# Performance work log

Hardware: AMD Instinct MI355X
Metric: run time of the kernel (lower is better)

The kernel has to match this reference:

```python
import jax, jax.numpy as jnp
from jax import lax
import numpy as np

B = 512      # instances
C = 64       # cases (segments)
HID = 1024
ATT = 128


def _conv(x, w, b):
    # torch Conv2d(kernel=5, padding=2), NCHW / OIHW layout
    y = lax.conv_general_dilated(x, w, (1, 1), [(2, 2), (2, 2)],
                                 dimension_numbers=('NCHW', 'OIHW', 'NCHW'))
    return y + b[None, :, None, None]


def _pool(x):
    # MaxPool2d(2)
    return lax.reduce_window(x, -jnp.inf, lax.max, (1, 1, 2, 2), (1, 1, 2, 2), 'VALID')


def setup_inputs() -> dict:
    key = jax.random.key(0)
    ks = jax.random.split(key, 20)

    def rn(k, shape, scale=0.05):
        return jax.random.normal(k, shape, dtype=jnp.float32) * scale

    inp = {
        'data': jax.random.normal(ks[0], (B, 3, 128, 128), dtype=jnp.float32),
        'case_ids': jnp.sort(jax.random.randint(ks[1], (B,), 0, C, dtype=jnp.int32)),
    }
    chans = [(3, 8), (8, 16), (16, 32), (32, 64), (64, 128)]
    for i, (ci, co) in enumerate(chans):
        inp[f'conv_w{i + 1}'] = rn(ks[2 + 2 * i], (co, ci, 5, 5))
        inp[f'conv_b{i + 1}'] = jnp.zeros((co,), jnp.float32)
    inp['fc_w'] = rn(ks[12], (HID, 128 * 4 * 4), 0.02)
    inp['fc_b'] = jnp.zeros((HID,), jnp.float32)
    inp['att_w1'] = rn(ks[13], (ATT, HID), 0.02)
    inp['att_b1'] = jnp.zeros((ATT,), jnp.float32)
    inp['att_w2'] = rn(ks[14], (1, ATT), 0.02)
    inp['att_b2'] = jnp.zeros((1,), jnp.float32)
    inp['clf_w'] = rn(ks[15], (1, HID), 0.02)
    inp['clf_b'] = jnp.zeros((1,), jnp.float32)
    return inp


def reference(data, case_ids, conv_w1, conv_b1, conv_w2, conv_b2, conv_w3, conv_b3,
              conv_w4, conv_b4, conv_w5, conv_b5, fc_w, fc_b,
              att_w1, att_b1, att_w2, att_b2, clf_w, clf_b):
    x = data
    for w, b in ((conv_w1, conv_b1), (conv_w2, conv_b2), (conv_w3, conv_b3),
                 (conv_w4, conv_b4), (conv_w5, conv_b5)):
        x = jax.nn.relu(_pool(_conv(x, w, b)))
    emb = x.reshape(x.shape[0], -1) @ fc_w.T + fc_b          # (B, HID)

    # --- segment (per-case) attention pooling, vectorized over all cases ---
    logits = (jnp.tanh(emb @ att_w1.T + att_b1) @ att_w2.T + att_b2)[:, 0]  # (B,)
    seg_max = jax.ops.segment_max(logits, case_ids, num_segments=C)
    seg_max = jnp.where(jnp.isfinite(seg_max), seg_max, 0.0)  # guard empty segments
    e = jnp.exp(logits - lax.stop_gradient(seg_max)[case_ids])
    denom = jax.ops.segment_sum(e, case_ids, num_segments=C)
    wgt = e / denom[case_ids]                                  # segment softmax
    aggr = jax.ops.segment_sum(wgt[:, None] * emb, case_ids, num_segments=C)  # (C, HID)

    # --- classifier ---
    return jax.nn.sigmoid(aggr @ clf_w.T + clf_b)              # (C, 1)
```

## Files before the change

### kernel.cpp

```cpp
#include <hip/hip_runtime.h>
#include <hip/hip_bf16.h>
#include <math.h>

#define BATCH 512
#define NSEG  64
#define HID   1024
#define ATT   128

typedef __attribute__((ext_vector_type(8))) __bf16 bf16x8;
typedef __attribute__((ext_vector_type(4))) __bf16 bf16x4;
typedef __attribute__((ext_vector_type(4))) float  f32x4;

__global__ void wconv1_k(const float* __restrict__ w, __bf16* __restrict__ wt) {
    int t = blockIdx.x * 256 + threadIdx.x;
    if (t >= 2048) return;
    int j = t & 7, m = (t >> 3) & 15, k8 = t >> 7;
    int k = k8 * 8 + j, tap = k >> 2, ci = k & 3;
    float v = 0.f;
    if (m < 8 && ci < 3 && tap < 25) v = w[(m * 3 + ci) * 25 + tap];
    wt[t] = (__bf16)v;
}

__global__ __launch_bounds__(256) void conv1_mfma_k(
    const float* __restrict__ in, const __bf16* __restrict__ Wt,
    const float* __restrict__ bias, __bf16* __restrict__ out) {
    constexpr int W  = 128;
    constexpr int R  = 4;
    constexpr int RP = R + 4;
    constexpr int WP = W + 4;
    constexpr int CSTR = R * W + 4;

    __shared__ __align__(16) __bf16 xs[RP * WP * 4];
    __shared__ float cs[8 * CSTR];

    const int tid = threadIdx.x;
    const int b   = blockIdx.x >> 5;
    const int y0  = (blockIdx.x & 31) * R;
    const float* inb = in + (size_t)b * 3 * 16384;

    if (tid < RP * 4) {
        int r = tid >> 2, s = tid & 3;
        int c = (s < 2) ? s : (128 + s);
        *(bf16x4*)(xs + (r * WP + c) * 4) = (bf16x4){};
    }
    {
        int r  = tid >> 5;
        int g  = tid & 31;
        int gy = y0 + r - 2;
        int c0 = g * 4;
        bf16x8 lo = {}, hi = {};
        if ((unsigned)gy < 128u) {
            const float* p = inb + (size_t)gy * 128 + c0;
            float4 a = *(const float4*)(p);
            float4 q = *(const float4*)(p + 16384);
            float4 c = *(const float4*)(p + 32768);
            lo[0] = (__bf16)a.x; lo[1] = (__bf16)q.x; lo[2] = (__bf16)c.x;
            lo[4] = (__bf16)a.y; lo[5] = (__bf16)q.y; lo[6] = (__bf16)c.y;
            hi[0] = (__bf16)a.z; hi[1] = (__bf16)q.z; hi[2] = (__bf16)c.z;
            hi[4] = (__bf16)a.w; hi[5] = (__bf16)q.w; hi[6] = (__bf16)c.w;
        }
        *(bf16x8*)(xs + (r * WP + c0 + 2) * 4)     = lo;
        *(bf16x8*)(xs + (r * WP + c0 + 2) * 4 + 8) = hi;
    }
    __syncthreads();

    const int lane = tid & 63, wave = tid >> 6;
    const int quad = lane >> 4, l15 = lane & 15;
    constexpr int F = 8;

    int pbase[F];
    f32x4 acc[F];
#pragma unroll
    for (int f = 0; f < F; ++f) {
        pbase[f] = ((wave + 2) * WP + f * 16 + l15 + 2) * 8;
        acc[f] = f32x4{0.f, 0.f, 0.f, 0.f};
    }
    const char* xsb = (const char*)xs;

#pragma unroll
    for (int kt = 0; kt < 4; ++kt) {
        int k8 = kt * 4 + quad;
        int tap0 = k8 * 2, tap1 = tap0 + 1;
        int t0 = tap0 < 25 ? tap0 : 0;
        int t1 = tap1 < 25 ? tap1 : 0;
        int s0 = ((t0 / 5 - 2) * WP + (t0 % 5 - 2)) * 8;
        int s1 = ((t1 / 5 - 2) * WP + (t1 % 5 - 2)) * 8;
        bf16x8 av = *(const bf16x8*)(Wt + ((size_t)k8 * 16 + l15) * 8);
#pragma unroll
        for (int f = 0; f < F; ++f) {
            bf16x4 b0 = *(const bf16x4*)(xsb + pbase[f] + s0);
            bf16x4 b1 = *(const bf16x4*)(xsb + pbase[f] + s1);
            bf16x8 bv = __builtin_shufflevector(b0, b1, 0, 1, 2, 3, 4, 5, 6, 7);
            acc[f] = __builtin_amdgcn_mfma_f32_16x16x32_bf16(av, bv, acc[f], 0, 0, 0);
        }
    }

#pragma unroll
    for (int f = 0; f < F; ++f) {
        int pl = wave * 128 + f * 16 + l15;
#pragma unroll
        for (int r = 0; r < 4; ++r) {
            int m = quad * 4 + r;
            if (m < 8) cs[m * CSTR + pl] = acc[f][r];
        }
    }
    __syncthreads();

    {
        int oi  = tid >> 1;
        int cog = (tid & 1) * 4;
        int oy  = oi >> 6, ox = oi & 63;
        int pl0 = oy * 2 * 128 + ox * 2;
        float4 b4 = *(const float4*)(bias + cog);
        bf16x4 ov;
#pragma unroll
        for (int i = 0; i < 4; ++i) {
            int cr = cog + i;
            float v0 = cs[cr * CSTR + pl0],       v1 = cs[cr * CSTR + pl0 + 1];
            float v2 = cs[cr * CSTR + pl0 + 128], v3 = cs[cr * CSTR + pl0 + 129];
            float m = fmaxf(fmaxf(v0, v1), fmaxf(v2, v3)) + ((const float*)&b4)[i];
            ov[i] = (__bf16)fmaxf(m, 0.f);
        }
        size_t ob = ((size_t)b * 4096 + (size_t)(y0 / 2 + oy) * 64 + ox) * 8 + cog;
        *(bf16x4*)(out + ob) = ov;
    }
}

template<int Ci, int Co>
__global__ void wconv_k(const float* __restrict__ w, __bf16* __restrict__ wt) {
    const int n = 25 * Ci * Co;
    int t = blockIdx.x * 256 + threadIdx.x;
    if (t >= n) return;
    int j  = t & 7;
    int t2 = t >> 3;
    int co = t2 % Co;
    int k8 = t2 / Co;
    int k  = k8 * 8 + j;
    int tap = k / Ci, ci = k % Ci;
    int kh = tap / 5, kw = tap % 5;
    wt[t] = (__bf16)w[((co * Ci + ci) * 25) + kh * 5 + kw];
}

__global__ void wfc_k(const float* __restrict__ w, __bf16* __restrict__ wt) {
    int t = blockIdx.x * 256 + threadIdx.x;
    int j  = t & 7;
    int t2 = t >> 3;
    int o  = t2 & 1023;
    int k8 = t2 >> 10;
    wt[t] = (__bf16)w[(size_t)o * 2048 + k8 * 8 + j];
}

template<int Ci, int Co, int H, int OUTMODE>
__global__ __launch_bounds__(256) void conv_mfma_k(
    const __bf16* __restrict__ X, const __bf16* __restrict__ Wt,
    const float* __restrict__ bias, void* __restrict__ outp) {
    constexpr int W = H, NPIX = H * W, NTOT = BATCH * NPIX;
    constexpr int HALO = 2 * W + 2, SPAN = 256 + 2 * HALO, STR = Ci + 8;
    constexpr int K = 25 * Ci, KT = (K + 31) / 32;
    constexpr int LOGW = (W == 64 ? 6 : (W == 32 ? 5 : (W == 16 ? 4 : 3)));

    __shared__ __align__(16) __bf16 xs[SPAN * STR];
    __shared__ float cs[16 * 256];

    const int tid  = threadIdx.x;
    const int pos0 = blockIdx.x * 256;
    const int co0  = blockIdx.y * 16;

    constexpr int C8 = Ci / 8;
    for (int i = tid; i < SPAN * C8; i += 256) {
        int p   = i / C8;
        int cio = (i % C8) * 8;
        int gp  = pos0 - HALO + p;
        gp = gp < 0 ? 0 : (gp > NTOT - 1 ? NTOT - 1 : gp);
        *(bf16x8*)(xs + p * STR + cio) = *(const bf16x8*)(X + (size_t)gp * Ci + cio);
    }
    __syncthreads();

    const int lane = tid & 63, wave = tid >> 6;
    const int quad = lane >> 4, l15 = lane & 15;

    int px[4], py[4], pbase[4];
    f32x4 acc[4];
#pragma unroll
    for (int f = 0; f < 4; ++f) {
        int pl = wave * 64 + f * 16 + l15;
        int p  = pos0 + pl;
        px[f] = p & (W - 1);
        py[f] = (p >> LOGW) & (H - 1);
        pbase[f] = (pl + HALO) * STR;
        acc[f] = f32x4{0.f, 0.f, 0.f, 0.f};
    }
    const bf16x8 BZ = {};

    for (int kt = 0; kt < KT; ++kt) {
        int k8 = kt * 4 + quad;
        int kk = k8 * 8;
        bool kok = kk < K;
        int kkc  = kok ? kk : 0;
        int tap  = kkc / Ci;
        int cib  = kkc % Ci;
        int dy   = tap / 5 - 2;
        int dx   = tap % 5 - 2;
        int shift = dy * W + dx;
        bf16x8 av = *(const bf16x8*)(Wt + ((size_t)(kok ? k8 : 0) * Co + co0 + l15) * 8);
#pragma unroll
        for (int f = 0; f < 4; ++f) {
            bf16x8 bv = *(const bf16x8*)(xs + pbase[f] + shift * STR + cib);
            bool valid = kok && ((unsigned)(px[f] + dx) < (unsigned)W)
                             && ((unsigned)(py[f] + dy) < (unsigned)H);
            if (!valid) bv = BZ;
            acc[f] = __builtin_amdgcn_mfma_f32_16x16x32_bf16(av, bv, acc[f], 0, 0, 0);
        }
    }

#pragma unroll
    for (int f = 0; f < 4; ++f) {
        int pl = wave * 64 + f * 16 + l15;
#pragma unroll
        for (int r = 0; r < 4; ++r) cs[(quad * 4 + r) * 256 + pl] = acc[f][r];
    }
    __syncthreads();

    {
        int opos = tid >> 2;
        int cog  = (tid & 3) * 4;
        int ocol = opos & (W / 2 - 1);
        int orow = opos >> (LOGW - 1);
        int pl0  = (orow * 2) * W + ocol * 2;
        int p    = pos0 + pl0;
        int b    = p >> (2 * LOGW);
        int yy   = (p >> LOGW) & (H - 1);
        int xx   = p & (W - 1);
        int oy = yy >> 1, ox = xx >> 1;
#pragma unroll
        for (int i = 0; i < 4; ++i) {
            int cr = cog + i;
            float v0 = cs[cr * 256 + pl0],     v1 = cs[cr * 256 + pl0 + 1];
            float v2 = cs[cr * 256 + pl0 + W], v3 = cs[cr * 256 + pl0 + W + 1];
            float m = fmaxf(fmaxf(v0, v1), fmaxf(v2, v3)) + bias[co0 + cr];
            m = fmaxf(m, 0.f);
            if (OUTMODE == 1) {
                ((__bf16*)outp)[(size_t)b * 2048 + (co0 + cr) * 16 + oy * 4 + ox] = (__bf16)m;
            } else {
                ((__bf16*)outp)[((size_t)((b * (H / 2) + oy) * (W / 2)) + ox) * Co + co0 + cr] = (__bf16)m;
            }
        }
    }
}

__global__ __launch_bounds__(256) void fc_mfma_k(
    const __bf16* __restrict__ Xb, const __bf16* __restrict__ Wfc,
    const float* __restrict__ bias, float* __restrict__ emb) {
    const int tid  = threadIdx.x;
    const int lane = tid & 63, wave = tid >> 6;
    const int quad = lane >> 4, l15 = lane & 15;
    const int n0   = blockIdx.x * 128;
    const int co0  = blockIdx.y * 16;

    int n[2];
    f32x4 acc[2];
#pragma unroll
    for (int f = 0; f < 2; ++f) {
        n[f] = n0 + wave * 32 + f * 16 + l15;
        acc[f] = f32x4{0.f, 0.f, 0.f, 0.f};
    }

#pragma unroll 4
    for (int kt = 0; kt < 64; ++kt) {
        int k8 = kt * 4 + quad;
        bf16x8 av = *(const bf16x8*)(Wfc + ((size_t)k8 * 1024 + co0 + l15) * 8);
#pragma unroll
        for (int f = 0; f < 2; ++f) {
            bf16x8 bv = *(const bf16x8*)(Xb + (size_t)n[f] * 2048 + k8 * 8);
            acc[f] = __builtin_amdgcn_mfma_f32_16x16x32_bf16(av, bv, acc[f], 0, 0, 0);
        }
    }

    float4 b4 = *(const float4*)(bias + co0 + quad * 4);
#pragma unroll
    for (int f = 0; f < 2; ++f) {
        f32x4 v = acc[f];
        v[0] += b4.x; v[1] += b4.y; v[2] += b4.z; v[3] += b4.w;
        *(f32x4*)(emb + (size_t)n[f] * 1024 + co0 + quad * 4) = v;
    }
}

__global__ __launch_bounds__(128) void attention_k(
    const float* __restrict__ emb, const float* __restrict__ w1,
    const float* __restrict__ b1, const float* __restrict__ w2,
    const float* __restrict__ b2, float* __restrict__ logits) {
    const int b = blockIdx.x;
    const int j = threadIdx.x;
    __shared__ float es[HID];
    for (int k = j; k < HID; k += 128) es[k] = emb[(size_t)b * HID + k];
    __syncthreads();

    float s = b1[j];
    const float* wr = w1 + (size_t)j * HID;
    for (int k = 0; k < HID; k += 4) {
        float4 wv = *(const float4*)(wr + k);
        float4 ev = *(const float4*)(es + k);
        s += wv.x * ev.x + wv.y * ev.y + wv.z * ev.z + wv.w * ev.w;
    }
    float v = tanhf(s) * w2[j];
#pragma unroll
    for (int off = 32; off > 0; off >>= 1) v += __shfl_down(v, off);
    __shared__ float wsum[2];
    if ((j & 63) == 0) wsum[j >> 6] = v;
    __syncthreads();
    if (j == 0) logits[b] = wsum[0] + wsum[1] + b2[0];
}

__global__ __launch_bounds__(256) void segment_k(
    const float* __restrict__ emb, const float* __restrict__ logits,
    const int* __restrict__ cid, const float* __restrict__ clf_w,
    const float* __restrict__ clf_b, float* __restrict__ out) {
    const int c = blockIdx.x;
    const int t = threadIdx.x;
    __shared__ int cids[BATCH];
    __shared__ float red[256];
    for (int i = t; i < BATCH; i += 256) cids[i] = cid[i];
    __syncthreads();

    float lm = -1e30f;
    for (int b = t; b < BATCH; b += 256)
        if (cids[b] == c) lm = fmaxf(lm, logits[b]);
    red[t] = lm; __syncthreads();
    for (int s = 128; s > 0; s >>= 1) {
        if (t < s) red[t] = fmaxf(red[t], red[t + s]);
        __syncthreads();
    }
    float smax = red[0]; __syncthreads();

    float ls = 0.f;
    for (int b = t; b < BATCH; b += 256)
        if (cids[b] == c) ls += expf(logits[b] - smax);
    red[t] = ls; __syncthreads();
    for (int s = 128; s > 0; s >>= 1) {
        if (t < s) red[t] += red[t + s];
        __syncthreads();
    }
    float denom = red[0]; __syncthreads();
    float inv = (denom > 0.f) ? 1.f / denom : 0.f;

    const int h0 = t * 4;
    float g0 = 0.f, g1 = 0.f, g2 = 0.f, g3 = 0.f;
    for (int b = 0; b < BATCH; ++b) {
        if (cids[b] == c) {
            float wgt = expf(logits[b] - smax) * inv;
            float4 ev = *(const float4*)(emb + (size_t)b * HID + h0);
            g0 = fmaf(wgt, ev.x, g0);
            g1 = fmaf(wgt, ev.y, g1);
            g2 = fmaf(wgt, ev.z, g2);
            g3 = fmaf(wgt, ev.w, g3);
        }
    }
    float4 cw = *(const float4*)(clf_w + h0);
    float ca = g0 * cw.x + g1 * cw.y + g2 * cw.z + g3 * cw.w;
    red[t] = ca; __syncthreads();
    for (int s = 128; s > 0; s >>= 1) {
        if (t < s) red[t] += red[t + s];
        __syncthreads();
    }
    if (t == 0) out[c] = 1.f / (1.f + expf(-(red[0] + clf_b[0])));
}

extern "C" void kernel_launch(void* const* d_in, const int* in_sizes, int n_in,
                              void* d_out, int out_size, void* d_ws, size_t ws_size,
                              hipStream_t stream) {
    const float* data = (const float*)d_in[0];
    const int*   cid  = (const int*)d_in[1];
    const float* cw1 = (const float*)d_in[2],  * cb1 = (const float*)d_in[3];
    const float* cw2 = (const float*)d_in[4],  * cb2 = (const float*)d_in[5];
    const float* cw3 = (const float*)d_in[6],  * cb3 = (const float*)d_in[7];
    const float* cw4 = (const float*)d_in[8],  * cb4 = (const float*)d_in[9];
    const float* cw5 = (const float*)d_in[10], * cb5 = (const float*)d_in[11];
    const float* fcw = (const float*)d_in[12], * fcb = (const float*)d_in[13];
    const float* aw1 = (const float*)d_in[14], * ab1 = (const float*)d_in[15];
    const float* aw2 = (const float*)d_in[16], * ab2 = (const float*)d_in[17];
    const float* clw = (const float*)d_in[18], * clb = (const float*)d_in[19];
    float* out = (float*)d_out;

    char* wsb = (char*)d_ws;
    __bf16* x1  = (__bf16*)(wsb);
    __bf16* x2  = (__bf16*)(wsb + 33554432);
    __bf16* x3  = (__bf16*)(wsb + 50331648);
    __bf16* x4  = (__bf16*)(wsb + 58720256);
    __bf16* x5b = (__bf16*)(wsb + 62914560);
    float*  emb = (float*) (wsb + 65011712);
    float*  lg  = (float*) (wsb + 67108864);
    __bf16* wt2 = (__bf16*)(wsb + 67110912);
    __bf16* wt3 = (__bf16*)(wsb + 67117312);
    __bf16* wt4 = (__bf16*)(wsb + 67142912);
    __bf16* wt5 = (__bf16*)(wsb + 67245312);
    __bf16* wfc = (__bf16*)(wsb + 67654912);
    __bf16* wt1 = (__bf16*)(wsb + 71849216);

    wconv1_k<<<8, 256, 0, stream>>>(cw1, wt1);
    wconv_k<8,  16 ><<<(3200   + 255) / 256, 256, 0, stream>>>(cw2, wt2);
    wconv_k<16, 32 ><<<(12800  + 255) / 256, 256, 0, stream>>>(cw3, wt3);
    wconv_k<32, 64 ><<<(51200  + 255) / 256, 256, 0, stream>>>(cw4, wt4);
    wconv_k<64, 128><<<(204800 + 255) / 256, 256, 0, stream>>>(cw5, wt5);
    wfc_k<<<2097152 / 256, 256, 0, stream>>>(fcw, wfc);

    conv1_mfma_k<<<16384, 256, 0, stream>>>(data, wt1, cb1, x1);

    conv_mfma_k<8,  16,  64, 0><<<dim3(8192, 1), 256, 0, stream>>>(x1, wt2, cb2, x2);
    conv_mfma_k<16, 32,  32, 0><<<dim3(2048, 2), 256, 0, stream>>>(x2, wt3, cb3, x3);
    conv_mfma_k<32, 64,  16, 0><<<dim3(512,  4), 256, 0, stream>>>(x3, wt4, cb4, x4);
    conv_mfma_k<64, 128, 8,  1><<<dim3(128,  8), 256, 0, stream>>>(x4, wt5, cb5, x5b);

    fc_mfma_k<<<dim3(4, 64), 256, 0, stream>>>(x5b, wfc, fcb, emb);
    attention_k<<<BATCH, 128, 0, stream>>>(emb, aw1, ab1, aw2, ab2, lg);
    segment_k<<<NSEG, 256, 0, stream>>>(emb, lg, cid, clw, clb, out);
}
```

Measured before the change: 435.0 us.

## Use 2D zero-padded shared tiles for conv layers, drop per-tap bounds checks

```diff
diff --git a/kernel.cpp b/kernel.cpp
--- a/kernel.cpp
+++ b/kernel.cpp
@@ -150,100 +150,134 @@
     wt[t] = (__bf16)w[(size_t)o * 2048 + k8 * 8 + j];
 }
 
-template<int Ci, int Co, int H, int OUTMODE>
-__global__ __launch_bounds__(256) void conv_mfma_k(
+template<int Ci, int Co, int H, int RB, int IMGS, int OUTMODE>
+__global__ __launch_bounds__(256) void conv2d_mfma_k(
     const __bf16* __restrict__ X, const __bf16* __restrict__ Wt,
     const float* __restrict__ bias, void* __restrict__ outp) {
-    constexpr int W = H, NPIX = H * W, NTOT = BATCH * NPIX;
-    constexpr int HALO = 2 * W + 2, SPAN = 256 + 2 * HALO, STR = Ci + 8;
-    constexpr int K = 25 * Ci, KT = (K + 31) / 32;
-    constexpr int LOGW = (W == 64 ? 6 : (W == 32 ? 5 : (W == 16 ? 4 : 3)));
-
-    __shared__ __align__(16) __bf16 xs[SPAN * STR];
-    __shared__ float cs[16 * 256];
-
-    const int tid  = threadIdx.x;
-    const int pos0 = blockIdx.x * 256;
-    const int co0  = blockIdx.y * 16;
-
-    constexpr int C8 = Ci / 8;
-    for (int i = tid; i < SPAN * C8; i += 256) {
-        int p   = i / C8;
-        int cio = (i % C8) * 8;
-        int gp  = pos0 - HALO + p;
-        gp = gp < 0 ? 0 : (gp > NTOT - 1 ? NTOT - 1 : gp);
-        *(bf16x8*)(xs + p * STR + cio) = *(const bf16x8*)(X + (size_t)gp * Ci + cio);
+    constexpr int W   = H;
+    constexpr int PW  = W + 4;
+    constexpr int PR  = RB + 4;
+    constexpr int PIX = RB * W;
+    constexpr int P   = IMGS * PIX;
+    constexpr int SE  = Ci + (Ci >= 16 ? 8 : 0);
+    constexpr int SB  = SE * 2;
+    constexpr int K   = 25 * Ci;
+    constexpr int KTF = K / 32;
+    constexpr int FW  = P / 64;
+    constexpr int PP  = P / 4;
+    constexpr int OW  = W / 2;
+    constexpr int CSTR = P + 1;
+    constexpr int C8  = Ci / 8;
+    constexpr int BPI = H / RB;
+
+    constexpr int XS_B = IMGS * PR * PW * SB;
+    constexpr int CS_B = 16 * CSTR * 4;
+    constexpr int SM_B = XS_B > CS_B ? XS_B : CS_B;
+    __shared__ __align__(16) char smem[SM_B];
+    __bf16* xs = (__bf16*)smem;
+    float*  cs = (float*)smem;
+
+    const int tid = threadIdx.x;
+    const int b0  = (blockIdx.x / BPI) * IMGS;
+    const int y0  = (blockIdx.x % BPI) * RB;
+    const int co0 = blockIdx.y * 16;
+
+    constexpr int NSLOT = IMGS * PR * PW * C8;
+    for (int i = tid; i < NSLOT; i += 256) {
+        int s   = i % C8;
+        int t2  = i / C8;
+        int pc  = t2 % PW;
+        int t3  = t2 / PW;
+        int pr  = t3 % PR;
+        int img = t3 / PR;
+        int gy  = y0 + pr - 2;
+        int gx  = pc - 2;
+        bf16x8 v = {};
+        if ((unsigned)gy < (unsigned)H && (unsigned)gx < (unsigned)W)
+            v = *(const bf16x8*)(X + (((size_t)(b0 + img) * H + gy) * W + gx) * Ci + s * 8);
+        *(bf16x8*)((char*)xs + ((size_t)(img * PR + pr) * PW + pc) * SB + s * 16) = v;
     }
     __syncthreads();
 
     const int lane = tid & 63, wave = tid >> 6;
     const int quad = lane >> 4, l15 = lane & 15;
 
-    int px[4], py[4], pbase[4];
-    f32x4 acc[4];
-#pragma unroll
-    for (int f = 0; f < 4; ++f) {
-        int pl = wave * 64 + f * 16 + l15;
-        int p  = pos0 + pl;
-        px[f] = p & (W - 1);
-        py[f] = (p >> LOGW) & (H - 1);
-        pbase[f] = (pl + HALO) * STR;
+    int pbase[FW];
+    f32x4 acc[FW];
+#pragma unroll
+    for (int f = 0; f < FW; ++f) {
+        int pos = (wave * FW + f) * 16 + l15;
+        int img = pos / PIX;
+        int r   = (pos & (PIX - 1)) / W;
+        int c   = pos & (W - 1);
+        pbase[f] = (img * PR + (r + 2)) * PW * SB + (c + 2) * SB;
         acc[f] = f32x4{0.f, 0.f, 0.f, 0.f};
     }
+    const char* xsb = (const char*)smem;
     const bf16x8 BZ = {};
 
-    for (int kt = 0; kt < KT; ++kt) {
-        int k8 = kt * 4 + quad;
-        int kk = k8 * 8;
-        bool kok = kk < K;
-        int kkc  = kok ? kk : 0;
-        int tap  = kkc / Ci;
-        int cib  = kkc % Ci;
-        int dy   = tap / 5 - 2;
-        int dx   = tap % 5 - 2;
-        int shift = dy * W + dx;
-        bf16x8 av = *(const bf16x8*)(Wt + ((size_t)(kok ? k8 : 0) * Co + co0 + l15) * 8);
-#pragma unroll
-        for (int f = 0; f < 4; ++f) {
-            bf16x8 bv = *(const bf16x8*)(xs + pbase[f] + shift * STR + cib);
-            bool valid = kok && ((unsigned)(px[f] + dx) < (unsigned)W)
-                             && ((unsigned)(py[f] + dy) < (unsigned)H);
-            if (!valid) bv = BZ;
+    auto body = [&](int kt, bool mask) {
+        int k8  = kt * 4 + quad;
+        int kk  = k8 * 8;
+        int kok = 1;
+        if (mask) { kok = kk < K; if (!kok) { k8 = 0; kk = 0; } }
+        int tap = kk / Ci, cio = kk % Ci;
+        int dy  = tap / 5 - 2, dx = tap % 5 - 2;
+        int shift = (dy * PW + dx) * SB + cio * 2;
+        bf16x8 av = *(const bf16x8*)(Wt + ((size_t)k8 * Co + co0 + l15) * 8);
+#pragma unroll
+        for (int f = 0; f < FW; ++f) {
+            bf16x8 bv = *(const bf16x8*)(xsb + pbase[f] + shift);
+            if (mask && !kok) bv = BZ;
             acc[f] = __builtin_amdgcn_mfma_f32_16x16x32_bf16(av, bv, acc[f], 0, 0, 0);
         }
-    }
-
-#pragma unroll
-    for (int f = 0; f < 4; ++f) {
-        int pl = wave * 64 + f * 16 + l15;
-#pragma unroll
-        for (int r = 0; r < 4; ++r) cs[(quad * 4 + r) * 256 + pl] = acc[f][r];
-    }
-    __syncthreads();
-
-    {
+    };
+#pragma unroll
+    for (int kt = 0; kt < KTF; ++kt) body(kt, false);
+    if constexpr (K % 32 != 0) body(KTF, true);
+
+    __syncthreads();
+#pragma unroll
+    for (int f = 0; f < FW; ++f) {
+        int pl = (wave * FW + f) * 16 + l15;
+#pragma unroll
+        for (int r = 0; r < 4; ++r) cs[(quad * 4 + r) * CSTR + pl] = acc[f][r];
+    }
+    __syncthreads();
+
+    constexpr int SLOTS = PP * 4;
+    if (tid < SLOTS) {
         int opos = tid >> 2;
         int cog  = (tid & 3) * 4;
-        int ocol = opos & (W / 2 - 1);
-        int orow = opos >> (LOGW - 1);
-        int pl0  = (orow * 2) * W + ocol * 2;
-        int p    = pos0 + pl0;
-        int b    = p >> (2 * LOGW);
-        int yy   = (p >> LOGW) & (H - 1);
-        int xx   = p & (W - 1);
-        int oy = yy >> 1, ox = xx >> 1;
+        constexpr int PPI = PIX / 4;
+        int img  = opos / PPI;
+        int rest = opos & (PPI - 1);
+        int oyl  = rest / OW;
+        int oxl  = rest & (OW - 1);
+        int pl0  = img * PIX + (oyl * 2) * W + oxl * 2;
+        int bb   = b0 + img;
+        int oy   = (y0 >> 1) + oyl;
+        float4 b4 = *(const float4*)(bias + co0 + cog);
+        float mv[4];
 #pragma unroll
         for (int i = 0; i < 4; ++i) {
             int cr = cog + i;
-            float v0 = cs[cr * 256 + pl0],     v1 = cs[cr * 256 + pl0 + 1];
-            float v2 = cs[cr * 256 + pl0 + W], v3 = cs[cr * 256 + pl0 + W + 1];
-            float m = fmaxf(fmaxf(v0, v1), fmaxf(v2, v3)) + bias[co0 + cr];
-            m = fmaxf(m, 0.f);
-            if (OUTMODE == 1) {
-                ((__bf16*)outp)[(size_t)b * 2048 + (co0 + cr) * 16 + oy * 4 + ox] = (__bf16)m;
-            } else {
-                ((__bf16*)outp)[((size_t)((b * (H / 2) + oy) * (W / 2)) + ox) * Co + co0 + cr] = (__bf16)m;
-            }
+            float v0 = cs[cr * CSTR + pl0],     v1 = cs[cr * CSTR + pl0 + 1];
+            float v2 = cs[cr * CSTR + pl0 + W], v3 = cs[cr * CSTR + pl0 + W + 1];
+            float m = fmaxf(fmaxf(v0, v1), fmaxf(v2, v3)) + ((const float*)&b4)[i];
+            mv[i] = fmaxf(m, 0.f);
+        }
+        if (OUTMODE == 1) {
+#pragma unroll
+            for (int i = 0; i < 4; ++i)
+                ((__bf16*)outp)[(size_t)bb * 2048 + (co0 + cog + i) * 16 + oy * 4 + oxl] =
+                    (__bf16)mv[i];
+        } else {
+            bf16x4 ov;
+#pragma unroll
+            for (int i = 0; i < 4; ++i) ov[i] = (__bf16)mv[i];
+            *(bf16x4*)((__bf16*)outp +
+                (((size_t)bb * (H / 2) + oy) * OW + oxl) * Co + co0 + cog) = ov;
         }
     }
 }
@@ -405,10 +439,10 @@
 
     conv1_mfma_k<<<16384, 256, 0, stream>>>(data, wt1, cb1, x1);
 
-    conv_mfma_k<8,  16,  64, 0><<<dim3(8192, 1), 256, 0, stream>>>(x1, wt2, cb2, x2);
-    conv_mfma_k<16, 32,  32, 0><<<dim3(2048, 2), 256, 0, stream>>>(x2, wt3, cb3, x3);
-    conv_mfma_k<32, 64,  16, 0><<<dim3(512,  4), 256, 0, stream>>>(x3, wt4, cb4, x4);
-    conv_mfma_k<64, 128, 8,  1><<<dim3(128,  8), 256, 0, stream>>>(x4, wt5, cb5, x5b);
+    conv2d_mfma_k<8,  16,  64, 4,  1, 0><<<dim3(512 * 16, 1), 256, 0, stream>>>(x1, wt2, cb2, x2);
+    conv2d_mfma_k<16, 32,  32, 8,  1, 0><<<dim3(512 * 4,  2), 256, 0, stream>>>(x2, wt3, cb3, x3);
+    conv2d_mfma_k<32, 64,  16, 16, 1, 0><<<dim3(512,      4), 256, 0, stream>>>(x3, wt4, cb4, x4);
+    conv2d_mfma_k<64, 128, 8,  8,  2, 1><<<dim3(256,      8), 256, 0, stream>>>(x4, wt5, cb5, x5b);
 
     fc_mfma_k<<<dim3(4, 64), 256, 0, stream>>>(x5b, wfc, fcb, emb);
     attention_k<<<BATCH, 128, 0, stream>>>(emb, aw1, ab1, aw2, ab2, lg);
```

New measurement: 433.7 us. Within noise of the previous version (-0.3%).
